# Performance work log

Measured on AMD Instinct MI355X. Metric: run time of the kernel, lower is better.

## Reference

```python
import jax, jax.numpy as jnp
import numpy as np

MAX_OOV = 100  # must match init_kwargs max_oov_size


def setup_inputs() -> dict:
    key = jax.random.key(0)
    k1, k2, k3, k4 = jax.random.split(key, 4)
    T, B, V, L = 32, 16, 50000, 400
    vocab_dists = jax.random.uniform(k1, (T, B, V), dtype=jnp.float32)
    attn_dists = jax.random.uniform(k2, (T, B, L), dtype=jnp.float32)
    p_gens = jax.random.uniform(k3, (T, B, 1), dtype=jnp.float32)
    input_ids = jax.random.randint(k4, (B, L), 0, V + MAX_OOV).astype(jnp.int64)
    return {"vocab_dists": vocab_dists, "attn_dists": attn_dists,
            "p_gens": p_gens, "input_ids": input_ids}


def reference(vocab_dists, attn_dists, p_gens, input_ids):
    # vocab_dists: [T, B, V], attn_dists: [T, B, L], p_gens: [T, B, 1]
    # input_ids: [B, L] with ids in [0, V + MAX_OOV)
    T, B, V = vocab_dists.shape
    L = attn_dists.shape[-1]
    ev = V + MAX_OOV  # extended vocab size

    # p_gen gating (fused elementwise)
    vd = p_gens * vocab_dists            # [T, B, V]
    ad = (1.0 - p_gens) * attn_dists     # [T, B, L]

    # extend generation dist with zeros for OOV slots
    vd_ext = jnp.pad(vd, ((0, 0), (0, 0), (0, MAX_OOV)))  # [T, B, ev]

    # scatter-add copy distribution into extended vocab (duplicates accumulate,
    # matching tf.scatter_nd semantics)
    rows = jnp.arange(B)[:, None]  # [B, 1] broadcast against input_ids [B, L]

    def scatter_one(a):  # a: [B, L] -> [B, ev]
        return jnp.zeros((B, ev), a.dtype).at[rows, input_ids].add(a)

    copy_proj = jax.vmap(scatter_one)(ad)  # [T, B, ev]

    return vd_ext + copy_proj  # [T, B, ev]
```

## Files before the change

### kernel.cpp

```cpp
#include <hip/hip_runtime.h>

#define TT 32
#define BB 16
#define VV 50000
#define LL 400
#define MAX_OOV 100
#define EV (VV + MAX_OOV)
#define EV4 (EV / 4)
#define V4 (VV / 4)

__global__ __launch_bounds__(256) void fdl_gate_kernel(
    const float* __restrict__ vocab,
    const float* __restrict__ pgen,
    float* __restrict__ out)
{
    const int row = blockIdx.y;
    const int i   = blockIdx.x * blockDim.x + threadIdx.x;
    if (i >= EV4) return;

    const float p = pgen[row];
    float4* __restrict__ o4 = reinterpret_cast<float4*>(out + (size_t)row * EV);

    if (i < V4) {
        const float4* __restrict__ v4 =
            reinterpret_cast<const float4*>(vocab + (size_t)row * VV);
        float4 v = v4[i];
        v.x *= p; v.y *= p; v.z *= p; v.w *= p;
        o4[i] = v;
    } else {
        o4[i] = make_float4(0.f, 0.f, 0.f, 0.f);
    }
}

__global__ __launch_bounds__(256) void fdl_scatter_kernel(
    const float* __restrict__ attn,
    const float* __restrict__ pgen,
    const int* __restrict__ ids,
    float* __restrict__ out)
{
    const int idx = blockIdx.x * blockDim.x + threadIdx.x;
    if (idx >= TT * BB * LL) return;

    const int l  = idx % LL;
    const int tb = idx / LL;
    const int b  = tb % BB;

    const float p = pgen[tb];
    const float a = attn[idx];
    const int   id = ids[b * LL + l];

    atomicAdd(out + (size_t)tb * EV + id, (1.0f - p) * a);
}

extern "C" void kernel_launch(void* const* d_in, const int* in_sizes, int n_in,
                              void* d_out, int out_size, void* d_ws, size_t ws_size,
                              hipStream_t stream) {
    const float* vocab = (const float*)d_in[0];
    const float* attn  = (const float*)d_in[1];
    const float* pgen  = (const float*)d_in[2];
    const int*   ids   = (const int*)d_in[3];
    float* out = (float*)d_out;

    dim3 gateGrid((EV4 + 255) / 256, TT * BB);
    fdl_gate_kernel<<<gateGrid, 256, 0, stream>>>(vocab, pgen, out);

    const int n_scatter = TT * BB * LL;
    fdl_scatter_kernel<<<(n_scatter + 255) / 256, 256, 0, stream>>>(
        attn, pgen, ids, out);
}
```

Baseline: 200.7 us.

## Fuse gating and scatter into one per-row kernel

```diff
diff --git a/kernel.cpp b/kernel.cpp
--- a/kernel.cpp
+++ b/kernel.cpp
@@ -7,49 +7,53 @@
 #define MAX_OOV 100
 #define EV (VV + MAX_OOV)
 #define EV4 (EV / 4)
-#define V4 (VV / 4)
+#define V4  (VV / 4)
+#define NTHREADS 512
+#define FULL_ITERS (V4 / NTHREADS)
 
-__global__ __launch_bounds__(256) void fdl_gate_kernel(
+__global__ __launch_bounds__(NTHREADS) void fdl_fused_kernel(
     const float* __restrict__ vocab,
+    const float* __restrict__ attn,
     const float* __restrict__ pgen,
+    const int*   __restrict__ ids,
     float* __restrict__ out)
 {
-    const int row = blockIdx.y;
-    const int i   = blockIdx.x * blockDim.x + threadIdx.x;
-    if (i >= EV4) return;
+    const int row = blockIdx.x;
+    const int tid = threadIdx.x;
+    const float p = pgen[row];
 
-    const float p = pgen[row];
-    float4* __restrict__ o4 = reinterpret_cast<float4*>(out + (size_t)row * EV);
+    const float4* __restrict__ v4 =
+        reinterpret_cast<const float4*>(vocab + (size_t)row * VV);
+    float4* __restrict__ o4 =
+        reinterpret_cast<float4*>(out + (size_t)row * EV);
 
-    if (i < V4) {
-        const float4* __restrict__ v4 =
-            reinterpret_cast<const float4*>(vocab + (size_t)row * VV);
+    int i = tid;
+    #pragma unroll 4
+    for (int it = 0; it < FULL_ITERS; ++it, i += NTHREADS) {
         float4 v = v4[i];
         v.x *= p; v.y *= p; v.z *= p; v.w *= p;
         o4[i] = v;
-    } else {
-        o4[i] = make_float4(0.f, 0.f, 0.f, 0.f);
     }
-}
+    if (i < V4) {
+        float4 v = v4[i];
+        v.x *= p; v.y *= p; v.z *= p; v.w *= p;
+        o4[i] = v;
+    }
+    if (tid < EV4 - V4) {
+        o4[V4 + tid] = make_float4(0.f, 0.f, 0.f, 0.f);
+    }
 
-__global__ __launch_bounds__(256) void fdl_scatter_kernel(
-    const float* __restrict__ attn,
-    const float* __restrict__ pgen,
-    const int* __restrict__ ids,
-    float* __restrict__ out)
-{
-    const int idx = blockIdx.x * blockDim.x + threadIdx.x;
-    if (idx >= TT * BB * LL) return;
+    __syncthreads();
 
-    const int l  = idx % LL;
-    const int tb = idx / LL;
-    const int b  = tb % BB;
+    const int b = row % BB;
+    const float q = 1.0f - p;
+    float* __restrict__ orow = out + (size_t)row * EV;
+    const float* __restrict__ arow = attn + (size_t)row * LL;
+    const int* __restrict__ irow = ids + (size_t)b * LL;
 
-    const float p = pgen[tb];
-    const float a = attn[idx];
-    const int   id = ids[b * LL + l];
-
-    atomicAdd(out + (size_t)tb * EV + id, (1.0f - p) * a);
+    if (tid < LL) {
+        atomicAdd(orow + irow[tid], q * arow[tid]);
+    }
 }
 
 extern "C" void kernel_launch(void* const* d_in, const int* in_sizes, int n_in,
@@ -61,10 +65,5 @@
     const int*   ids   = (const int*)d_in[3];
     float* out = (float*)d_out;
 
-    dim3 gateGrid((EV4 + 255) / 256, TT * BB);
-    fdl_gate_kernel<<<gateGrid, 256, 0, stream>>>(vocab, pgen, out);
-
-    const int n_scatter = TT * BB * LL;
-    fdl_scatter_kernel<<<(n_scatter + 255) / 256, 256, 0, stream>>>(
-        attn, pgen, ids, out);
+    fdl_fused_kernel<<<TT * BB, NTHREADS, 0, stream>>>(vocab, attn, pgen, ids, out);
 }
```

New measurement: 205.1 us. +2.2%, slower.
